# Kernel tuning notes

Measured on AMD Instinct MI355X. Metric: run time of the kernel, lower is better.

## Reference

```python
import jax, jax.numpy as jnp
import numpy as np

X, U, AD, H = 32, 8, 24, 256
T, B = 128, 256
MIN_V, MAX_V = 0.01, 1.0
EPS = 1e-6


def setup_inputs() -> dict:
    key = jax.random.key(0)
    ks = jax.random.split(key, 10)
    s = lambda k, sh: jax.random.normal(k, sh, jnp.float32) * 0.05
    return {
        "u": jax.random.normal(ks[0], (T, B, U), jnp.float32),
        "a": jax.random.normal(ks[1], (T, B, AD), jnp.float32),
        "W1": s(ks[2], (H, X)), "b1": jnp.zeros((H,), jnp.float32),
        "W2": s(ks[3], (H, H)), "b2": jnp.zeros((H,), jnp.float32),
        "WA": s(ks[4], (X * X, H)), "bA": jnp.zeros((X * X,), jnp.float32),
        "WB": s(ks[5], (X * U, H)), "bB": jnp.zeros((X * U,), jnp.float32),
        "WC": s(ks[6], (AD * X, H)), "bC": jnp.zeros((AD * X,), jnp.float32),
        "Wnx": s(ks[7], (X, H)), "bnx": jnp.zeros((X,), jnp.float32),
        "Wna": s(ks[8], (AD, H)), "bna": jnp.zeros((AD,), jnp.float32),
        "alpha": jnp.array([0.01], jnp.float32),
    }


def _forward(u, a, W1, b1, W2, b2, WA, bA, WB, bB, WC, bC, Wnx, bnx, Wna, bna, alpha):
    eyeX = jnp.eye(X, dtype=u.dtype)
    eyeA = jnp.eye(AD, dtype=u.dtype)

    def dyn(x):
        # locally-linear dynamics heads; x: [B, X]
        h = jax.nn.relu(x @ W1.T + b1)
        h = jax.nn.relu(h @ W2.T + b2)
        b = x.shape[0]
        Am = eyeX + alpha[0] * (h @ WA.T + bA).reshape(b, X, X)
        Bm = (h @ WB.T + bB).reshape(b, X, U)
        Cm = (h @ WC.T + bC).reshape(b, AD, X)
        nx = MIN_V + (MAX_V - MIN_V) * jax.nn.sigmoid(h @ Wnx.T + bnx)
        na = MIN_V + (MAX_V - MIN_V) * jax.nn.sigmoid(h @ Wna.T + bna)
        return Am, Bm, Cm, nx, na

    def make_psd(P):
        return 0.5 * (P + jnp.swapaxes(P, -1, -2)) + EPS * eyeX

    def prior_step(mean, cov, u_t):
        Am, Bm, _, nx, _ = dyn(mean)
        nm = jnp.einsum('bij,bj->bi', Am, mean) + jnp.einsum('bij,bj->bi', Bm, u_t)
        nc = jnp.einsum('bij,bjk,blk->bil', Am, cov, Am) + nx[:, :, None] * eyeX
        return nm, make_psd(nc)

    def post_step(mean, cov, a_t):
        _, _, Cm, _, na = dyn(mean)
        S = jnp.einsum('bij,bjk,blk->bil', Cm, cov, Cm) + na[:, :, None] * eyeA
        Sp = jnp.linalg.pinv(S)
        G = jnp.einsum('bij,bkj,bkl->bil', cov, Cm, Sp)  # cov @ C^T @ pinv(S)
        innov = a_t - jnp.einsum('bij,bj->bi', Cm, mean)
        nm = mean + jnp.einsum('bij,bj->bi', G, innov)
        nc = cov - jnp.einsum('bij,bjk,bkl->bil', G, Cm, cov)
        return nm, make_psd(nc)

    pm0 = jnp.zeros((B, X), u.dtype)
    pc0 = jnp.broadcast_to(eyeX, (B, X, X))
    qm0, qc0 = post_step(pm0, pc0, a[0])

    def step(carry, inp):
        qm, qc = carry
        u_t, a_next = inp
        prm, prc = prior_step(qm, qc, u_t)
        nqm, nqc = post_step(prm, prc, a_next)
        return (nqm, nqc), (prm, prc, nqm, nqc)

    _, (prm, prc, qm, qc) = jax.lax.scan(step, (qm0, qc0), (u[:-1], a[1:]))
    prior_means = jnp.concatenate([pm0[None], prm], axis=0)
    prior_covs = jnp.concatenate([pc0[None], prc], axis=0)
    post_means = jnp.concatenate([qm0[None], qm], axis=0)
    post_covs = jnp.concatenate([qc0[None], qc], axis=0)
    return prior_means, prior_covs, post_means, post_covs


def reference(u, a, W1, b1, W2, b2, WA, bA, WB, bB, WC, bC, Wnx, bnx, Wna, bna, alpha):
    return _forward(u, a, W1, b1, W2, b2, WA, bA, WB, bB, WC, bC, Wnx, bnx, Wna, bna, alpha)
```

## Files before the change

kernel.cpp:

```cpp
#include <hip/hip_runtime.h>
#include <hip/hip_bf16.h>
#include <math.h>

typedef unsigned int uint32;
typedef _Float16 h2_t __attribute__((ext_vector_type(2)));

static constexpr int NX = 32;
static constexpr int NU = 8;
static constexpr int NA = 24;
static constexpr int NH = 256;
static constexpr int NT = 128;
static constexpr int NB = 256;
static constexpr int NXP = 33;
static constexpr float MINV = 0.01f, MAXV = 1.0f, EPSV = 1e-6f;

static constexpr int H1O = NX*NX + NX*NU + NX;
static constexpr int H1P = 1344;
static constexpr int H2O = NA*NX + NA;
static constexpr int H2P = 800;

static constexpr size_t OFF_W1 = 0;
static constexpr size_t OFF_W2 = 4096;
static constexpr size_t OFF_H1 = OFF_W2 + 32768;
static constexpr size_t OFF_H2 = OFF_H1 + 172032;
static constexpr size_t OFF_B1 = OFF_H2 + 102400;
static constexpr size_t OFF_B2 = OFF_B1 + 1344;

__global__ void pack_half_off(const float* __restrict__ src, uint32* __restrict__ dst,
                              int O, int K, int LDP, int off)
{
    int idx = blockIdx.x * blockDim.x + threadIdx.x;
    int K2 = K >> 1;
    if (idx >= O * K2) return;
    int kk = idx % K2;
    int o  = idx / K2;
    int k  = kk * 2;
    int k8 = k >> 3, q = (k >> 1) & 3;
    _Float16 a = (_Float16)src[o * K + k];
    _Float16 b = (_Float16)src[o * K + k + 1];
    uint32 val = (uint32)__builtin_bit_cast(unsigned short, a)
               | ((uint32)__builtin_bit_cast(unsigned short, b) << 16);
    dst[((size_t)k8 * LDP + off + o) * 4 + q] = val;
}

__global__ void pack_bias3(const float* __restrict__ s0, int n0,
                           const float* __restrict__ s1, int n1,
                           const float* __restrict__ s2, int n2,
                           float* __restrict__ dst)
{
    int i = blockIdx.x * blockDim.x + threadIdx.x;
    if (i < n0) dst[i] = s0[i];
    else if (i < n0 + n1) dst[i] = s1[i - n0];
    else if (i < n0 + n1 + n2) dst[i] = s2[i - n0 - n1];
}

__device__ __forceinline__ float dot2(uint32 w, uint32 x, float acc)
{
#if __has_builtin(__builtin_amdgcn_fdot2)
    return __builtin_amdgcn_fdot2(__builtin_bit_cast(h2_t, w),
                                  __builtin_bit_cast(h2_t, x), acc, false);
#else
    h2_t a = __builtin_bit_cast(h2_t, w), b = __builtin_bit_cast(h2_t, x);
    return acc + (float)a[0] * (float)b[0] + (float)a[1] * (float)b[1];
#endif
}

__device__ __forceinline__ float dot8(uint4 w, uint4 x, float acc)
{
    acc = dot2(w.x, x.x, acc);
    acc = dot2(w.y, x.y, acc);
    acc = dot2(w.z, x.z, acc);
    acc = dot2(w.w, x.w, acc);
    return acc;
}

__device__ __forceinline__ void tri_decode(int p, int& l, int& i)
{
    int lo = (int)((sqrtf(8.f * (float)p + 1.f) - 1.f) * 0.5f);
    while ((lo + 1) * (lo + 2) / 2 <= p) lo++;
    while (lo * (lo + 1) / 2 > p) lo--;
    l = lo;
    i = p - lo * (lo + 1) / 2;
}

__device__ __forceinline__ float sigm_scaled(float z)
{
    return MINV + (MAXV - MINV) / (1.f + expf(-z));
}

__device__ __forceinline__ unsigned short f2h(float v)
{
    _Float16 h = (_Float16)v;
    return __builtin_bit_cast(unsigned short, h);
}

__device__ __forceinline__ void pack1_to(int tid, float v, uint32* d)
{
    unsigned short us = f2h(v);
    int pi = __shfl_xor((int)us, 1);
    if ((tid & 1) == 0)
        d[tid >> 1] = (uint32)us | ((uint32)pi << 16);
}

__device__ __forceinline__ void bar()
{
    asm volatile("s_waitcnt lgkmcnt(0)" ::: "memory");
    __builtin_amdgcn_s_barrier();
    asm volatile("" ::: "memory");
}

__global__ __launch_bounds__(1024, 4) void kf_kernel(
    const float* __restrict__ u, const float* __restrict__ a,
    const uint32* __restrict__ wsu,
    const float* __restrict__ b1, const float* __restrict__ b2,
    const float* __restrict__ alpha_p,
    float* __restrict__ out)
{
    const int tid = threadIdx.x;
    const int b   = blockIdx.x;
    const float alpha = alpha_p[0];

    const uint4* W1h = (const uint4*)(wsu + OFF_W1);
    const uint4* W2h = (const uint4*)(wsu + OFF_W2);
    const uint4* H1h = (const uint4*)(wsu + OFF_H1);
    const uint4* H2h = (const uint4*)(wsu + OFF_H2);
    const float* BH1 = (const float*)(wsu + OFF_B1);
    const float* BH2 = (const float*)(wsu + OFF_B2);

    __shared__ alignas(16) uint4 s_w2[8 * 1024];

    __shared__ alignas(16) uint32 s_h1h[NH / 2];
    __shared__ alignas(16) uint32 s_h2h[NH / 2];
    __shared__ alignas(16) uint32 s_qmh[NX / 2];
    __shared__ alignas(16) uint32 s_pmh[NX / 2];
    __shared__ alignas(16) float s_Am[NX * NXP];
    __shared__ float s_Bm[NX * NU];
    __shared__ float s_nx[NX];
    __shared__ alignas(16) float s_C[NA * NXP];
    __shared__ float s_na[NA];
    __shared__ float s_qm[NX];
    __shared__ alignas(16) float s_qc[NX * NXP];
    __shared__ float s_pm[NX];
    __shared__ alignas(16) float s_pc[NX * NXP];
    __shared__ alignas(16) float s_T2[NX * NXP];
    __shared__ alignas(16) float s_T1[NA * NXP];
    __shared__ float s_S[NA * NA];
    __shared__ float s_Y[NA * NX];
    __shared__ float s_innov[NA];
    __shared__ float s_a[NA], s_u[NU];

    const size_t pmO = 0;
    const size_t pcO = (size_t)NT * NB * NX;
    const size_t qmO = pcO + (size_t)NT * NB * NX * NX;
    const size_t qcO = qmO + (size_t)NT * NB * NX;

    {
        const int o = tid >> 2, g = tid & 3;
        #pragma unroll
        for (int kk = 0; kk < 8; kk++)
            s_w2[kk * 1024 + tid] = W2h[(g * 8 + kk) * NH + o];
    }

    const float b1v  = (tid < NH) ? b1[tid] : 0.f;
    const float b2v  = b2[tid >> 2];
    const float bh1a = BH1[tid];
    const float bh1b = (tid + 1024 < H1O) ? BH1[tid + 1024] : 0.f;
    const float bh2v = (tid < H2P) ? BH2[tid] : 0.f;

    int iT = 0, lT = 0;
    if (tid >= 256 && tid < 784) tri_decode(tid - 256, lT, iT);
    int iS = 0, lS = 0;
    if (tid < 300) tri_decode(tid, lS, iS);

    for (int t = 0; t < NT; ++t) {
        const size_t mIdx = (size_t)t * NB + b;

        if (t == 0) {
            if (tid < NX) s_pm[tid] = 0.f;
            if (tid < NX / 2) s_pmh[tid] = 0u;
            {
                int i = tid >> 5, l = tid & 31;
                s_pc[i * NXP + l] = (i == l) ? 1.f : 0.f;
            }
            bar();
        } else {
            const size_t mPrev = (size_t)(t - 1) * NB + b;

            if (tid < NH) {
                const uint4* xh = (const uint4*)s_qmh;
                float acc = b1v;
                #pragma unroll
                for (int k8 = 0; k8 < 4; k8++)
                    acc = dot8(W1h[k8 * NH + tid], xh[k8], acc);
                pack1_to(tid, fmaxf(acc, 0.f), s_h1h);
            } else if (tid < 784) {
                const int i = iT, l = lT;
                float t_il = 0.f, t_li = 0.f;
                #pragma unroll
                for (int q = 0; q < NA; q++) {
                    t_il = fmaf(s_Y[q * NX + i], s_T1[q * NXP + l], t_il);
                    t_li = fmaf(s_Y[q * NX + l], s_T1[q * NXP + i], t_li);
                }
                if (i == l) {
                    s_qc[i * NXP + i] = s_pc[i * NXP + i] - t_il + EPSV;
                } else {
                    float v = 0.5f * ((s_pc[i * NXP + l] - t_il) + (s_pc[l * NXP + i] - t_li));
                    s_qc[i * NXP + l] = v;
                    s_qc[l * NXP + i] = v;
                }
            } else if (tid < 816) {
                __builtin_nontemporal_store(s_qm[tid - 784], out + qmO + mPrev * NX + (tid - 784));
            } else if (tid < 824) {
                s_u[tid - 816] = u[mPrev * NU + (tid - 816)];
            }
            bar();

            {
                __builtin_nontemporal_store(s_qc[(tid >> 5) * NXP + (tid & 31)],
                                            out + qcO + mPrev * (NX * NX) + tid);
                const uint4* xh = (const uint4*)s_h1h;
                float acc = 0.f;
                #pragma unroll
                for (int kk = 0; kk < 8; kk++)
                    acc = dot8(s_w2[kk * 1024 + tid], xh[(tid & 3) * 8 + kk], acc);
                acc += __shfl_xor(acc, 1);
                acc += __shfl_xor(acc, 2);
                float v = fmaxf(acc + b2v, 0.f);
                unsigned short us = f2h(v);
                int pi = __shfl_xor((int)us, 4);
                if ((tid & 7) == 0) s_h2h[tid >> 3] = (uint32)us | ((uint32)pi << 16);
            }
            bar();

            {
                const uint4* xh = (const uint4*)s_h2h;
                int o0 = tid, o1 = tid + 1024;
                float a0 = bh1a;
                float a1 = bh1b;
                #pragma unroll 8
                for (int k8 = 0; k8 < 32; k8++) {
                    uint4 x = xh[k8];
                    a0 = dot8(H1h[k8 * H1P + o0], x, a0);
                    if (o1 < H1O) a1 = dot8(H1h[k8 * H1P + o1], x, a1);
                }
                {
                    int i = o0 >> 5, l = o0 & 31;
                    s_Am[i * NXP + l] = ((i == l) ? 1.f : 0.f) + alpha * a0;
                }
                if (o1 < H1O) {
                    if (o1 < NX * NX + NX * NU) s_Bm[o1 - NX * NX] = a1;
                    else s_nx[o1 - (NX * NX + NX * NU)] = sigm_scaled(a1);
                }
            }
            bar();

            {
                int i = tid >> 5, l = tid & 31;
                float acc = 0.f;
                #pragma unroll
                for (int j = 0; j < NX; j++)
                    acc = fmaf(s_Am[i * NXP + j], s_qc[j * NXP + l], acc);
                s_T2[i * NXP + l] = acc;
            }
            if (tid < NX) {
                float acc = 0.f;
                #pragma unroll
                for (int j = 0; j < NX; j++) acc = fmaf(s_Am[tid * NXP + j], s_qm[j], acc);
                #pragma unroll
                for (int j = 0; j < NU; j++) acc = fmaf(s_Bm[tid * NU + j], s_u[j], acc);
                s_pm[tid] = acc;
                pack1_to(tid, acc, s_pmh);
            }
            bar();
        }

        if (tid < NH) {
            const uint4* xh = (const uint4*)s_pmh;
            float acc = b1v;
            #pragma unroll
            for (int k8 = 0; k8 < 4; k8++)
                acc = dot8(W1h[k8 * NH + tid], xh[k8], acc);
            pack1_to(tid, fmaxf(acc, 0.f), s_h1h);
        } else if (tid < 784) {
            if (t > 0) {
                const int i = iT, l = lT;
                float a_il = 0.f, a_li = 0.f;
                #pragma unroll
                for (int j = 0; j < NX; j++) {
                    a_il = fmaf(s_T2[i * NXP + j], s_Am[l * NXP + j], a_il);
                    a_li = fmaf(s_T2[l * NXP + j], s_Am[i * NXP + j], a_li);
                }
                if (i == l) {
                    s_pc[i * NXP + i] = a_il + s_nx[i] + EPSV;
                } else {
                    float v = 0.5f * (a_il + a_li);
                    s_pc[i * NXP + l] = v;
                    s_pc[l * NXP + i] = v;
                }
            }
        } else if (tid < 816) {
            __builtin_nontemporal_store(s_pm[tid - 784], out + pmO + mIdx * NX + (tid - 784));
        } else if (tid < 840) {
            s_a[tid - 816] = a[mIdx * NA + (tid - 816)];
        }
        bar();

        {
            __builtin_nontemporal_store(s_pc[(tid >> 5) * NXP + (tid & 31)],
                                        out + pcO + mIdx * (NX * NX) + tid);
            const uint4* xh = (const uint4*)s_h1h;
            float acc = 0.f;
            #pragma unroll
            for (int kk = 0; kk < 8; kk++)
                acc = dot8(s_w2[kk * 1024 + tid], xh[(tid & 3) * 8 + kk], acc);
            acc += __shfl_xor(acc, 1);
            acc += __shfl_xor(acc, 2);
            float v = fmaxf(acc + b2v, 0.f);
            unsigned short us = f2h(v);
            int pi = __shfl_xor((int)us, 4);
            if ((tid & 7) == 0) s_h2h[tid >> 3] = (uint32)us | ((uint32)pi << 16);
        }
        bar();

        if (tid < H2P) {
            const uint4* xh = (const uint4*)s_h2h;
            float acc = bh2v;
            #pragma unroll 8
            for (int k8 = 0; k8 < 32; k8++)
                acc = dot8(H2h[k8 * H2P + tid], xh[k8], acc);
            if (tid < NA * NX) {
                int i = tid >> 5, l = tid & 31;
                s_C[i * NXP + l] = acc;
            } else if (tid < H2O) {
                s_na[tid - NA * NX] = sigm_scaled(acc);
            }
        }
        bar();

        if (tid < NA * NX) {
            int i = tid >> 5, l = tid & 31;
            float acc = 0.f;
            #pragma unroll
            for (int k = 0; k < NX; k++)
                acc = fmaf(s_C[i * NXP + k], s_pc[k * NXP + l], acc);
            s_T1[i * NXP + l] = acc;
        } else if (tid < NA * NX + NA) {
            int i = tid - NA * NX;
            float acc = s_a[i];
            #pragma unroll
            for (int j = 0; j < NX; j++)
                acc = fmaf(-s_C[i * NXP + j], s_pm[j], acc);
            s_innov[i] = acc;
        }
        bar();

        if (tid < 300) {
            float acc = 0.f;
            #pragma unroll
            for (int j = 0; j < NX; j++)
                acc = fmaf(s_T1[iS * NXP + j], s_C[lS * NXP + j], acc);
            if (iS == lS) acc += s_na[iS];
            s_S[iS * NA + lS] = acc;
            s_S[lS * NA + iS] = acc;
        }
        bar();

        if (tid < 64) {
            const int j = tid;
            float r[NA];
            #pragma unroll
            for (int i = 0; i < NA; i++) {
                float v = 0.f;
                if (j < NA) v = s_S[i * NA + j];
                else if (j < NA + NX) v = s_T1[i * NXP + (j - NA)];
                r[i] = v;
            }
            #pragma unroll
            for (int k = 0; k < NA; k++) {
                float piv = __shfl(r[k], k);
                float ip = 1.0f / piv;
                r[k] *= ip;
                #pragma unroll
                for (int i = 0; i < NA; i++) {
                    if (i == k) continue;
                    float f = __shfl(r[i], k);
                    r[i] = fmaf(-f, r[k], r[i]);
                }
            }
            if (j >= NA && j < NA + NX) {
                const int x = j - NA;
                float acc = s_pm[x];
                #pragma unroll
                for (int i = 0; i < NA; i++) {
                    s_Y[i * NX + x] = r[i];
                    acc = fmaf(r[i], s_innov[i], acc);
                }
                s_qm[x] = acc;
                unsigned short us = f2h(acc);
                int pi = __shfl_xor((int)us, 1);
                if ((x & 1) == 0) s_qmh[x >> 1] = (uint32)us | ((uint32)pi << 16);
            }
        }
        asm volatile("s_waitcnt vmcnt(0)" ::: "memory");
        bar();
    }

    if (tid >= 256 && tid < 784) {
        const int i = iT, l = lT;
        float t_il = 0.f, t_li = 0.f;
        #pragma unroll
        for (int q = 0; q < NA; q++) {
            t_il = fmaf(s_Y[q * NX + i], s_T1[q * NXP + l], t_il);
            t_li = fmaf(s_Y[q * NX + l], s_T1[q * NXP + i], t_li);
        }
        if (i == l) {
            s_qc[i * NXP + i] = s_pc[i * NXP + i] - t_il + EPSV;
        } else {
            float v = 0.5f * ((s_pc[i * NXP + l] - t_il) + (s_pc[l * NXP + i] - t_li));
            s_qc[i * NXP + l] = v;
            s_qc[l * NXP + i] = v;
        }
    }
    bar();
    {
        const size_t mLast = (size_t)(NT - 1) * NB + b;
        for (int s = tid; s < NX + NX * NX; s += 1024) {
            if (s < NX)
                __builtin_nontemporal_store(s_qm[s], out + qmO + mLast * NX + s);
            else {
                int o = s - NX, i = o >> 5, l = o & 31;
                __builtin_nontemporal_store(s_qc[i * NXP + l],
                                            out + qcO + mLast * NX * NX + o);
            }
        }
    }
}

extern "C" void kernel_launch(void* const* d_in, const int* in_sizes, int n_in,
                              void* d_out, int out_size, void* d_ws, size_t ws_size,
                              hipStream_t stream)
{
    const float* u    = (const float*)d_in[0];
    const float* a    = (const float*)d_in[1];
    const float* W1   = (const float*)d_in[2];
    const float* b1   = (const float*)d_in[3];
    const float* W2   = (const float*)d_in[4];
    const float* b2   = (const float*)d_in[5];
    const float* WA   = (const float*)d_in[6];
    const float* bA   = (const float*)d_in[7];
    const float* WB   = (const float*)d_in[8];
    const float* bB   = (const float*)d_in[9];
    const float* WC   = (const float*)d_in[10];
    const float* bC   = (const float*)d_in[11];
    const float* Wnx  = (const float*)d_in[12];
    const float* bnx  = (const float*)d_in[13];
    const float* Wna  = (const float*)d_in[14];
    const float* bna  = (const float*)d_in[15];
    const float* alph = (const float*)d_in[16];

    uint32* wsu = (uint32*)d_ws;
    float* out = (float*)d_out;

    auto pk = [&](const float* src, int O, int K, size_t dst_off, int LDP, int off) {
        int n = O * (K / 2);
        pack_half_off<<<(n + 255) / 256, 256, 0, stream>>>(src, wsu + dst_off, O, K, LDP, off);
    };
    pk(W1,  NH,      NX, OFF_W1, NH,  0);
    pk(W2,  NH,      NH, OFF_W2, NH,  0);
    pk(WA,  NX * NX, NH, OFF_H1, H1P, 0);
    pk(WB,  NX * NU, NH, OFF_H1, H1P, NX * NX);
    pk(Wnx, NX,      NH, OFF_H1, H1P, NX * NX + NX * NU);
    pk(WC,  NA * NX, NH, OFF_H2, H2P, 0);
    pk(Wna, NA,      NH, OFF_H2, H2P, NA * NX);

    pack_bias3<<<(H1O + 255) / 256, 256, 0, stream>>>(bA, NX * NX, bB, NX * NU, bnx, NX,
                                                      (float*)(wsu + OFF_B1));
    pack_bias3<<<(H2O + 255) / 256, 256, 0, stream>>>(bC, NA * NX, bna, NA, nullptr, 0,
                                                      (float*)(wsu + OFF_B2));

    kf_kernel<<<NB, 1024, 0, stream>>>(u, a, wsu, b1, b2, alph, out);
}
```

Baseline: 3.665 ms.

## Transpose shared-memory operands for float2 reads and rebalance head matvec work

Pads rows to 34 floats and keeps transposed copies of Y and T1 in a scratch buffer. This lets the small matrix products read contiguous rows as float2 loads instead of strided scalar loads. The h1 vector gets per-64 padding to avoid LDS bank conflicts, and each block rotates the start of its k-loop in the weight matvecs so blocks read different global rows at the same time. The tail outputs of the first head (Bm and nx) are now split across thread pairs with a shuffle reduction instead of being handled by the first few threads alone. The cost is more LDS traffic for the scratch copies and more index arithmetic, and scratch reuse between the T2 and transposed-T1 phases must stay correctly ordered by barriers.

New measurement: 3.992 ms. 8.9% more time.

```diff
diff --git a/kernel.cpp b/kernel.cpp
--- a/kernel.cpp
+++ b/kernel.cpp
@@ -11,7 +11,8 @@
 static constexpr int NH = 256;
 static constexpr int NT = 128;
 static constexpr int NB = 256;
-static constexpr int NXP = 33;
+static constexpr int NXP = 34;
+static constexpr int NAT = 26;
 static constexpr float MINV = 0.01f, MAXV = 1.0f, EPSV = 1e-6f;
 
 static constexpr int H1O = NX*NX + NX*NU + NX;
@@ -102,6 +103,14 @@
         d[tid >> 1] = (uint32)us | ((uint32)pi << 16);
 }
 
+__device__ __forceinline__ void pack1_h1(int tid, float v, uint32* d)
+{
+    unsigned short us = f2h(v);
+    int pi = __shfl_xor((int)us, 1);
+    if ((tid & 1) == 0)
+        d[(tid >> 1) + ((tid >> 6) << 2)] = (uint32)us | ((uint32)pi << 16);
+}
+
 __device__ __forceinline__ void bar()
 {
     asm volatile("s_waitcnt lgkmcnt(0)" ::: "memory");
@@ -119,6 +128,7 @@
     const int tid = threadIdx.x;
     const int b   = blockIdx.x;
     const float alpha = alpha_p[0];
+    const int rot = (b >> 3) & 31;
 
     const uint4* W1h = (const uint4*)(wsu + OFF_W1);
     const uint4* W2h = (const uint4*)(wsu + OFF_W2);
@@ -129,25 +139,26 @@
 
     __shared__ alignas(16) uint4 s_w2[8 * 1024];
 
-    __shared__ alignas(16) uint32 s_h1h[NH / 2];
+    __shared__ alignas(16) uint32 s_h1h[144];
     __shared__ alignas(16) uint32 s_h2h[NH / 2];
     __shared__ alignas(16) uint32 s_qmh[NX / 2];
     __shared__ alignas(16) uint32 s_pmh[NX / 2];
     __shared__ alignas(16) float s_Am[NX * NXP];
-    __shared__ float s_Bm[NX * NU];
-    __shared__ float s_nx[NX];
+    __shared__ alignas(16) float s_Bm[NX * NU];
+    __shared__ alignas(16) float s_nx[NX];
     __shared__ alignas(16) float s_C[NA * NXP];
-    __shared__ float s_na[NA];
-    __shared__ float s_qm[NX];
+    __shared__ alignas(16) float s_na[NA];
+    __shared__ alignas(16) float s_qm[NX];
     __shared__ alignas(16) float s_qc[NX * NXP];
-    __shared__ float s_pm[NX];
+    __shared__ alignas(16) float s_pm[NX];
     __shared__ alignas(16) float s_pc[NX * NXP];
-    __shared__ alignas(16) float s_T2[NX * NXP];
+    __shared__ alignas(16) float s_scr[NX * NXP];
     __shared__ alignas(16) float s_T1[NA * NXP];
-    __shared__ float s_S[NA * NA];
-    __shared__ float s_Y[NA * NX];
-    __shared__ float s_innov[NA];
-    __shared__ float s_a[NA], s_u[NU];
+    __shared__ alignas(16) float s_S[NA * NA];
+    __shared__ alignas(16) float s_Yt[NX * NAT];
+    __shared__ alignas(16) float s_innov[NA];
+    __shared__ alignas(16) float s_a[NA];
+    __shared__ alignas(16) float s_u[NU];
 
     const size_t pmO = 0;
     const size_t pcO = (size_t)NT * NB * NX;
@@ -164,7 +175,7 @@
     const float b1v  = (tid < NH) ? b1[tid] : 0.f;
     const float b2v  = b2[tid >> 2];
     const float bh1a = BH1[tid];
-    const float bh1b = (tid + 1024 < H1O) ? BH1[tid + 1024] : 0.f;
+    const float bh1t = (tid >= 448) ? BH1[1024 + ((tid - 448) >> 1)] : 0.f;
     const float bh2v = (tid < H2P) ? BH2[tid] : 0.f;
 
     int iT = 0, lT = 0;
@@ -192,14 +203,22 @@
                 #pragma unroll
                 for (int k8 = 0; k8 < 4; k8++)
                     acc = dot8(W1h[k8 * NH + tid], xh[k8], acc);
-                pack1_to(tid, fmaxf(acc, 0.f), s_h1h);
+                pack1_h1(tid, fmaxf(acc, 0.f), s_h1h);
             } else if (tid < 784) {
                 const int i = iT, l = lT;
+                const float2* yi = (const float2*)&s_Yt[i * NAT];
+                const float2* tl = (const float2*)&s_scr[l * NAT];
+                const float2* yl = (const float2*)&s_Yt[l * NAT];
+                const float2* ti = (const float2*)&s_scr[i * NAT];
                 float t_il = 0.f, t_li = 0.f;
                 #pragma unroll
-                for (int q = 0; q < NA; q++) {
-                    t_il = fmaf(s_Y[q * NX + i], s_T1[q * NXP + l], t_il);
-                    t_li = fmaf(s_Y[q * NX + l], s_T1[q * NXP + i], t_li);
+                for (int q2 = 0; q2 < NA / 2; q2++) {
+                    float2 ya = yi[q2], ta = tl[q2];
+                    t_il = fmaf(ya.x, ta.x, t_il);
+                    t_il = fmaf(ya.y, ta.y, t_il);
+                    float2 yb = yl[q2], tb = ti[q2];
+                    t_li = fmaf(yb.x, tb.x, t_li);
+                    t_li = fmaf(yb.y, tb.y, t_li);
                 }
                 if (i == l) {
                     s_qc[i * NXP + i] = s_pc[i * NXP + i] - t_il + EPSV;
@@ -222,7 +241,7 @@
                 float acc = 0.f;
                 #pragma unroll
                 for (int kk = 0; kk < 8; kk++)
-                    acc = dot8(s_w2[kk * 1024 + tid], xh[(tid & 3) * 8 + kk], acc);
+                    acc = dot8(s_w2[kk * 1024 + tid], xh[(tid & 3) * 9 + kk], acc);
                 acc += __shfl_xor(acc, 1);
                 acc += __shfl_xor(acc, 2);
                 float v = fmaxf(acc + b2v, 0.f);
@@ -234,33 +253,49 @@
 
             {
                 const uint4* xh = (const uint4*)s_h2h;
-                int o0 = tid, o1 = tid + 1024;
                 float a0 = bh1a;
-                float a1 = bh1b;
                 #pragma unroll 8
-                for (int k8 = 0; k8 < 32; k8++) {
-                    uint4 x = xh[k8];
-                    a0 = dot8(H1h[k8 * H1P + o0], x, a0);
-                    if (o1 < H1O) a1 = dot8(H1h[k8 * H1P + o1], x, a1);
+                for (int k8r = 0; k8r < 32; k8r++) {
+                    int k8 = (k8r + rot) & 31;
+                    a0 = dot8(H1h[k8 * H1P + tid], xh[k8], a0);
+                }
+                float a1tot = 0.f;
+                int o1 = 0;
+                if (tid >= 448) {
+                    int tau = tid - 448;
+                    o1 = 1024 + (tau >> 1);
+                    int g = tau & 1;
+                    float a1 = g ? 0.f : bh1t;
+                    #pragma unroll 8
+                    for (int kk = 0; kk < 16; kk++) {
+                        int k8 = (g * 16 + kk + rot) & 31;
+                        a1 = dot8(H1h[k8 * H1P + o1], xh[k8], a1);
+                    }
+                    a1tot = a1 + __shfl_xor(a1, 1);
                 }
                 {
-                    int i = o0 >> 5, l = o0 & 31;
+                    int i = tid >> 5, l = tid & 31;
                     s_Am[i * NXP + l] = ((i == l) ? 1.f : 0.f) + alpha * a0;
                 }
-                if (o1 < H1O) {
-                    if (o1 < NX * NX + NX * NU) s_Bm[o1 - NX * NX] = a1;
-                    else s_nx[o1 - (NX * NX + NX * NU)] = sigm_scaled(a1);
+                if (tid >= 448 && ((tid - 448) & 1) == 0) {
+                    if (o1 < NX * NX + NX * NU) s_Bm[o1 - NX * NX] = a1tot;
+                    else s_nx[o1 - (NX * NX + NX * NU)] = sigm_scaled(a1tot);
                 }
             }
             bar();
 
             {
                 int i = tid >> 5, l = tid & 31;
+                const float2* amr = (const float2*)&s_Am[i * NXP];
+                const float2* qcr = (const float2*)&s_qc[l * NXP];
                 float acc = 0.f;
                 #pragma unroll
-                for (int j = 0; j < NX; j++)
-                    acc = fmaf(s_Am[i * NXP + j], s_qc[j * NXP + l], acc);
-                s_T2[i * NXP + l] = acc;
+                for (int j2 = 0; j2 < NX / 2; j2++) {
+                    float2 am = amr[j2], qc = qcr[j2];
+                    acc = fmaf(am.x, qc.x, acc);
+                    acc = fmaf(am.y, qc.y, acc);
+                }
+                s_scr[i * NXP + l] = acc;
             }
             if (tid < NX) {
                 float acc = 0.f;
@@ -280,15 +315,23 @@
             #pragma unroll
             for (int k8 = 0; k8 < 4; k8++)
                 acc = dot8(W1h[k8 * NH + tid], xh[k8], acc);
-            pack1_to(tid, fmaxf(acc, 0.f), s_h1h);
+            pack1_h1(tid, fmaxf(acc, 0.f), s_h1h);
         } else if (tid < 784) {
             if (t > 0) {
                 const int i = iT, l = lT;
+                const float2* t2i = (const float2*)&s_scr[i * NXP];
+                const float2* t2l = (const float2*)&s_scr[l * NXP];
+                const float2* ami = (const float2*)&s_Am[i * NXP];
+                const float2* aml = (const float2*)&s_Am[l * NXP];
                 float a_il = 0.f, a_li = 0.f;
                 #pragma unroll
-                for (int j = 0; j < NX; j++) {
-                    a_il = fmaf(s_T2[i * NXP + j], s_Am[l * NXP + j], a_il);
-                    a_li = fmaf(s_T2[l * NXP + j], s_Am[i * NXP + j], a_li);
+                for (int j2 = 0; j2 < NX / 2; j2++) {
+                    float2 p = t2i[j2], q = aml[j2];
+                    a_il = fmaf(p.x, q.x, a_il);
+                    a_il = fmaf(p.y, q.y, a_il);
+                    float2 r2 = t2l[j2], s2 = ami[j2];
+                    a_li = fmaf(r2.x, s2.x, a_li);
+                    a_li = fmaf(r2.y, s2.y, a_li);
                 }
                 if (i == l) {
                     s_pc[i * NXP + i] = a_il + s_nx[i] + EPSV;
@@ -312,7 +355,7 @@
             float acc = 0.f;
             #pragma unroll
             for (int kk = 0; kk < 8; kk++)
-                acc = dot8(s_w2[kk * 1024 + tid], xh[(tid & 3) * 8 + kk], acc);
+                acc = dot8(s_w2[kk * 1024 + tid], xh[(tid & 3) * 9 + kk], acc);
             acc += __shfl_xor(acc, 1);
             acc += __shfl_xor(acc, 2);
             float v = fmaxf(acc + b2v, 0.f);
@@ -326,8 +369,10 @@
             const uint4* xh = (const uint4*)s_h2h;
             float acc = bh2v;
             #pragma unroll 8
-            for (int k8 = 0; k8 < 32; k8++)
+            for (int k8r = 0; k8r < 32; k8r++) {
+                int k8 = (k8r + rot) & 31;
                 acc = dot8(H2h[k8 * H2P + tid], xh[k8], acc);
+            }
             if (tid < NA * NX) {
                 int i = tid >> 5, l = tid & 31;
                 s_C[i * NXP + l] = acc;
@@ -339,26 +384,42 @@
 
         if (tid < NA * NX) {
             int i = tid >> 5, l = tid & 31;
+            const float2* cr = (const float2*)&s_C[i * NXP];
+            const float2* pr = (const float2*)&s_pc[l * NXP];
             float acc = 0.f;
             #pragma unroll
-            for (int k = 0; k < NX; k++)
-                acc = fmaf(s_C[i * NXP + k], s_pc[k * NXP + l], acc);
+            for (int k2 = 0; k2 < NX / 2; k2++) {
+                float2 c = cr[k2], p = pr[k2];
+                acc = fmaf(c.x, p.x, acc);
+                acc = fmaf(c.y, p.y, acc);
+            }
             s_T1[i * NXP + l] = acc;
+            s_scr[l * NAT + i] = acc;
         } else if (tid < NA * NX + NA) {
             int i = tid - NA * NX;
+            const float2* cr = (const float2*)&s_C[i * NXP];
+            const float2* pm2 = (const float2*)s_pm;
             float acc = s_a[i];
             #pragma unroll
-            for (int j = 0; j < NX; j++)
-                acc = fmaf(-s_C[i * NXP + j], s_pm[j], acc);
+            for (int j2 = 0; j2 < NX / 2; j2++) {
+                float2 c = cr[j2], p = pm2[j2];
+                acc = fmaf(-c.x, p.x, acc);
+                acc = fmaf(-c.y, p.y, acc);
+            }
             s_innov[i] = acc;
         }
         bar();
 
         if (tid < 300) {
+            const float2* t1 = (const float2*)&s_T1[iS * NXP];
+            const float2* cl = (const float2*)&s_C[lS * NXP];
             float acc = 0.f;
             #pragma unroll
-            for (int j = 0; j < NX; j++)
-                acc = fmaf(s_T1[iS * NXP + j], s_C[lS * NXP + j], acc);
+            for (int j2 = 0; j2 < NX / 2; j2++) {
+                float2 x = t1[j2], y = cl[j2];
+                acc = fmaf(x.x, y.x, acc);
+                acc = fmaf(x.y, y.y, acc);
+            }
             if (iS == lS) acc += s_na[iS];
             s_S[iS * NA + lS] = acc;
             s_S[lS * NA + iS] = acc;
@@ -392,7 +453,7 @@
                 float acc = s_pm[x];
                 #pragma unroll
                 for (int i = 0; i < NA; i++) {
-                    s_Y[i * NX + x] = r[i];
+                    s_Yt[x * NAT + i] = r[i];
                     acc = fmaf(r[i], s_innov[i], acc);
                 }
                 s_qm[x] = acc;
@@ -410,8 +471,8 @@
         float t_il = 0.f, t_li = 0.f;
         #pragma unroll
         for (int q = 0; q < NA; q++) {
-            t_il = fmaf(s_Y[q * NX + i], s_T1[q * NXP + l], t_il);
-            t_li = fmaf(s_Y[q * NX + l], s_T1[q * NXP + i], t_li);
+            t_il = fmaf(s_Yt[i * NAT + q], s_scr[l * NAT + q], t_il);
+            t_li = fmaf(s_Yt[l * NAT + q], s_scr[i * NAT + q], t_li);
         }
         if (i == l) {
             s_qc[i * NXP + i] = s_pc[i * NXP + i] - t_il + EPSV;
```
